# Kernel tuning notes

Hardware: AMD Instinct MI355X
Metric: run time of the kernel (lower is better)

Reference implementation:

```python
import jax, jax.numpy as jnp
import numpy as np

EPS = 1e-8
LAMBDA_LSE = 6.0
LAMBDA_SOFTMAX = 9.0
LEAKY_SLOPE = 0.1


def setup_inputs() -> dict:
    key = jax.random.key(0)
    k1, k2, k3 = jax.random.split(key, 3)
    images = jax.random.normal(k1, (128, 36, 512), dtype=jnp.float32)
    captions = jax.random.normal(k2, (64, 32, 512), dtype=jnp.float32)
    # caption lengths in [4, 32] so no caption is empty
    cap_lens = jax.random.randint(k3, (64,), 4, 33, dtype=jnp.int64)
    return {"images": images, "captions": captions, "cap_lens": cap_lens}


def reference(images, captions, cap_lens):
    """Vectorized xattn_score_t2i with raw_feature_norm='clipped_l2norm',
    agg_func='LogSumExp'. images: (I,R,D); captions: (C,L,D); cap_lens: (C,).
    Returns similarities (I, C), matching the torch per-caption loop.
    """
    C, L, D = captions.shape
    mask = jnp.arange(L)[None, :] < cap_lens[:, None]          # (C, L)

    # attn = bmm(context=images, query^T=words): (C, I, R, L)
    attn = jnp.einsum('ird,cld->cirl', images, captions)
    attn = jax.nn.leaky_relu(attn, LEAKY_SLOPE)
    # zero out padded words; equivalent to slicing caption to cap_len
    attn = attn * mask[:, None, None, :]
    # l2norm along the word dim (dim=2 of (I,R,L) in original)
    norm = jnp.sqrt(jnp.sum(attn * attn, axis=-1, keepdims=True)) + EPS
    attn = attn / norm

    # transpose -> (C, I, L, R); softmax over regions with smoothing
    attn = jnp.swapaxes(attn, -1, -2)
    attn = jax.nn.softmax(attn * LAMBDA_SOFTMAX, axis=-1)

    # weighted context: (C, I, L, D)
    wctx = jnp.einsum('cilr,ird->cild', attn, images)

    # cosine similarity between caption words and weighted context over D
    cap = captions[:, None, :, :]                               # (C, 1, L, D)
    num = jnp.sum(cap * wctx, axis=-1)                          # (C, I, L)
    den = (jnp.maximum(jnp.linalg.norm(cap, axis=-1), EPS) *
           jnp.maximum(jnp.linalg.norm(wctx, axis=-1), EPS))
    row_sim = num / den                                         # (C, I, L)

    # LogSumExp aggregation over valid words
    scores = jnp.where(mask[:, None, :], row_sim * LAMBDA_LSE, -jnp.inf)
    sims = jax.nn.logsumexp(scores, axis=-1) / LAMBDA_LSE       # (C, I)
    return sims.T                                               # (I, C)
```

## Files before the change

### kernel.cpp

```cpp
#include <hip/hip_runtime.h>
#include <math.h>

constexpr int In = 128, Rn = 36, Cn = 64, Ln = 32, Dn = 512;
constexpr int Mn = In * Rn;
constexpr int Nn = Cn * Ln;
constexpr size_t ABOFF = 0;
constexpr size_t BBOFF = (size_t)Mn * Dn / 2;
constexpr size_t GBOFF = BBOFF + (size_t)Nn * Dn / 2;
constexpr size_t CNOFF = GBOFF + (size_t)In * 48 * 64 / 2;
constexpr size_t WSFLOATS = CNOFF + (size_t)Cn * Ln;
constexpr float EPSf = 1e-8f, LLSE = 6.0f, LSM = 9.0f, SLOPE = 0.1f;

using short8 = __attribute__((ext_vector_type(8))) short;
using f32x4  = __attribute__((ext_vector_type(4))) float;

__device__ __forceinline__ float dot4(float4 a, float4 b) {
  return a.x * b.x + a.y * b.y + a.z * b.z + a.w * b.w;
}

__device__ __forceinline__ unsigned short f2bf(float x) {
  union { float f; unsigned u; } v; v.f = x;
  unsigned r = v.u + 0x7fffu + ((v.u >> 16) & 1u);
  return (unsigned short)(r >> 16);
}

__device__ __forceinline__ short8 pack8(float4 u, float4 v) {
  short8 s;
  s[0] = (short)f2bf(u.x); s[1] = (short)f2bf(u.y); s[2] = (short)f2bf(u.z); s[3] = (short)f2bf(u.w);
  s[4] = (short)f2bf(v.x); s[5] = (short)f2bf(v.y); s[6] = (short)f2bf(v.z); s[7] = (short)f2bf(v.w);
  return s;
}

extern "C" __global__ __launch_bounds__(256, 2)
void scan_pre(const float* __restrict__ images, const float* __restrict__ captions,
              float* __restrict__ ws)
{
  __shared__ unsigned short sI[48 * 520];
  const int tid = threadIdx.x;
  const int bx = blockIdx.x;
  const short8 z8 = {0, 0, 0, 0, 0, 0, 0, 0};

  if (bx < 128) {
    const int i = bx;
    const float* gi = images + (size_t)i * Rn * Dn;
    unsigned short* Ab = (unsigned short*)(ws + ABOFF) + (size_t)i * Rn * Dn;
    for (int q = 0; q < 9; ++q) {
      int ch = tid + q * 256;
      int r = ch >> 6, c8 = (ch & 63) * 8;
      float4 u = *reinterpret_cast<const float4*>(gi + r * Dn + c8);
      float4 v = *reinterpret_cast<const float4*>(gi + r * Dn + c8 + 4);
      short8 p = pack8(u, v);
      *reinterpret_cast<short8*>(Ab + r * Dn + c8) = p;
      *reinterpret_cast<short8*>(&sI[r * 520 + c8]) = p;
    }
    for (int q = 0; q < 3; ++q) {
      int ch = tid + q * 256;
      int r = 36 + (ch >> 6), c8 = (ch & 63) * 8;
      *reinterpret_cast<short8*>(&sI[r * 520 + c8]) = z8;
    }
    __syncthreads();
    const int lane = tid & 63, wv = tid >> 6;
    const int lr = lane & 15, lk = lane >> 4;
    unsigned short* gb = (unsigned short*)(ws + GBOFF) + (size_t)i * 48 * 64;
    for (int t = wv; t < 9; t += 4) {
      const int mt = t / 3, nt = t - mt * 3;
      f32x4 acc = {0.f, 0.f, 0.f, 0.f};
      for (int k = 0; k < 16; ++k) {
        short8 af = *reinterpret_cast<const short8*>(&sI[(mt * 16 + lr) * 520 + k * 32 + lk * 8]);
        short8 bf = *reinterpret_cast<const short8*>(&sI[(nt * 16 + lr) * 520 + k * 32 + lk * 8]);
        acc = __builtin_amdgcn_mfma_f32_16x16x32_bf16(af, bf, acc, 0, 0, 0);
      }
      #pragma unroll
      for (int j = 0; j < 4; ++j)
        gb[(mt * 16 + lk * 4 + j) * 64 + nt * 16 + lr] = f2bf(acc[j]);
    }
    if (tid < 96) {
      int r = tid >> 1, h = tid & 1;
      *reinterpret_cast<short8*>(gb + r * 64 + 48 + h * 8) = z8;
    }
    return;
  }
  if (bx < 640) {
    const int chunk = (bx - 128) * 256 + tid;
    const int c  = chunk >> 11;
    const int cc = chunk & 2047;
    const int ln = cc & 63;
    const int fc = cc >> 6;
    const int t  = fc >> 2;
    const int ks = (fc >> 1) & 1;
    const int y  = fc & 1;
    const int lr = ln & 15, lk = ln >> 4;
    const float* src = captions + ((size_t)c * Ln + y * 16 + lr) * Dn
                     + t * 64 + ks * 32 + lk * 8;
    float4 u = *reinterpret_cast<const float4*>(src);
    float4 v = *reinterpret_cast<const float4*>(src + 4);
    unsigned short* dst = (unsigned short*)(ws + BBOFF) + (size_t)chunk * 8;
    *reinterpret_cast<short8*>(dst) = pack8(u, v);
    return;
  }
  {
    const int c = bx - 640;
    const float* gc = captions + (size_t)c * Ln * Dn;
    const int l = tid >> 3, p = tid & 7;
    float s = 0.f;
    #pragma unroll
    for (int t = 0; t < 16; ++t) {
      float4 v = *reinterpret_cast<const float4*>(gc + l * Dn + p * 64 + t * 4);
      s += dot4(v, v);
    }
    s += __shfl_xor(s, 1, 64); s += __shfl_xor(s, 2, 64); s += __shfl_xor(s, 4, 64);
    if (p == 0) ws[CNOFF + c * Ln + l] = s;
  }
}

extern "C" __global__ __launch_bounds__(256, 3)
void scan_fused(const float* __restrict__ ws, const int* __restrict__ cap_lens,
                float* __restrict__ out)
{
  __shared__ unsigned short sA[48 * 520];
  const unsigned short* Ab = (const unsigned short*)(ws + ABOFF);
  const unsigned short* Bf = (const unsigned short*)(ws + BBOFF);
  const unsigned short* GbAll = (const unsigned short*)(ws + GBOFF);
  const float* cnArr = ws + CNOFF;

  const int tid = threadIdx.x;
  int bid = blockIdx.x;
  bid = (bid & 7) * 256 + (bid >> 3);
  const int ig = bid >> 4;
  const int cg = bid & 15;
  const int lane = tid & 63, wv = tid >> 6;
  const int lr = lane & 15, lk = lane >> 4;
  const int cap = cg * 4 + wv;
  const int len = cap_lens[cap];
  const short8 z8 = {0, 0, 0, 0, 0, 0, 0, 0};

  {
    const unsigned short* Abi = Ab + (size_t)ig * (Rn * Dn);
    #pragma unroll
    for (int q = 0; q < 9; ++q) {
      int ch = tid + q * 256;
      int r = ch >> 6, c8 = (ch & 63) * 8;
      *reinterpret_cast<short8*>(&sA[r * 520 + c8]) =
        *reinterpret_cast<const short8*>(Abi + r * Dn + c8);
    }
    #pragma unroll
    for (int q = 0; q < 3; ++q) {
      int ch = tid + q * 256;
      int r = 36 + (ch >> 6), c8 = (ch & 63) * 8;
      *reinterpret_cast<short8*>(&sA[r * 520 + c8]) = z8;
    }
  }
  __syncthreads();

  const unsigned short* gBp = Bf + (size_t)cap * 16384 + lane * 8;
  const unsigned short* rA = &sA[lr * 520 + lk * 8];

  f32x4 acc[3][2];
  #pragma unroll
  for (int x = 0; x < 3; ++x)
    #pragma unroll
    for (int y = 0; y < 2; ++y) acc[x][y] = {0.f, 0.f, 0.f, 0.f};

  short8 bc[4], bn[4];
  #pragma unroll
  for (int f = 0; f < 4; ++f)
    bc[f] = *reinterpret_cast<const short8*>(gBp + f * 512);

  #pragma unroll 2
  for (int t = 0; t < 8; ++t) {
    if (t < 7) {
      #pragma unroll
      for (int f = 0; f < 4; ++f)
        bn[f] = *reinterpret_cast<const short8*>(gBp + (t + 1) * 2048 + f * 512);
    }
    #pragma unroll
    for (int ks = 0; ks < 2; ++ks) {
      short8 af[3];
      #pragma unroll
      for (int x = 0; x < 3; ++x)
        af[x] = *reinterpret_cast<const short8*>(rA + x * 8320 + t * 64 + ks * 32);
      #pragma unroll
      for (int x = 0; x < 3; ++x)
        #pragma unroll
        for (int y = 0; y < 2; ++y)
          acc[x][y] = __builtin_amdgcn_mfma_f32_16x16x32_bf16(af[x], bc[ks * 2 + y], acc[x][y], 0, 0, 0);
    }
    if (t < 7) {
      #pragma unroll
      for (int f = 0; f < 4; ++f) bc[f] = bn[f];
    }
  }

  const unsigned short* Gb = GbAll + (size_t)ig * 48 * 64;
  short8 gfr[3][2];
  #pragma unroll
  for (int x = 0; x < 3; ++x)
    #pragma unroll
    for (int ks = 0; ks < 2; ++ks)
      gfr[x][ks] = *reinterpret_cast<const short8*>(Gb + (x * 16 + lr) * 64 + ks * 32 + lk * 8);
  const float cn0 = cnArr[cap * 32 + lr];
  const float cn1 = cnArr[cap * 32 + 16 + lr];

  float s[3][2][4];
  #pragma unroll
  for (int x = 0; x < 3; ++x)
    #pragma unroll
    for (int y = 0; y < 2; ++y) {
      const int l = y * 16 + lr;
      #pragma unroll
      for (int j = 0; j < 4; ++j) {
        float v = acc[x][y][j];
        v = v > 0.f ? v : SLOPE * v;
        if (l >= len) v = 0.f;
        s[x][y][j] = v;
      }
    }

  float zinv[3][4];
  #pragma unroll
  for (int x = 0; x < 3; ++x)
    #pragma unroll
    for (int j = 0; j < 4; ++j) {
      float t = s[x][0][j] * s[x][0][j] + s[x][1][j] * s[x][1][j];
      t += __shfl_xor(t, 1, 64); t += __shfl_xor(t, 2, 64);
      t += __shfl_xor(t, 4, 64); t += __shfl_xor(t, 8, 64);
      zinv[x][j] = LSM / (sqrtf(t) + EPSf);
    }

  const bool x2ok = (lk == 0);
  float mcol[2] = {-1e30f, -1e30f};
  #pragma unroll
  for (int x = 0; x < 3; ++x)
    #pragma unroll
    for (int y = 0; y < 2; ++y)
      #pragma unroll
      for (int j = 0; j < 4; ++j) {
        float zz = s[x][y][j] * zinv[x][j];
        s[x][y][j] = zz;
        if (x < 2 || x2ok) mcol[y] = fmaxf(mcol[y], zz);
      }
  #pragma unroll
  for (int y = 0; y < 2; ++y) {
    mcol[y] = fmaxf(mcol[y], __shfl_xor(mcol[y], 16, 64));
    mcol[y] = fmaxf(mcol[y], __shfl_xor(mcol[y], 32, 64));
  }

  float e[3][2][4];
  float esum[2] = {0.f, 0.f}, num[2] = {0.f, 0.f};
  #pragma unroll
  for (int x = 0; x < 3; ++x)
    #pragma unroll
    for (int y = 0; y < 2; ++y)
      #pragma unroll
      for (int j = 0; j < 4; ++j) {
        float ev = (x < 2 || x2ok) ? __expf(s[x][y][j] - mcol[y]) : 0.f;
        e[x][y][j] = ev;
        esum[y] += ev;
        num[y] = fmaf(ev, acc[x][y][j], num[y]);
      }
  #pragma unroll
  for (int y = 0; y < 2; ++y) {
    esum[y] += __shfl_xor(esum[y], 16, 64); esum[y] += __shfl_xor(esum[y], 32, 64);
    num[y]  += __shfl_xor(num[y], 16, 64);  num[y]  += __shfl_xor(num[y], 32, 64);
  }

  __syncthreads();
  unsigned short* ET = &sA[36 * 520 + wv * 1552];
  #pragma unroll
  for (int x = 0; x < 3; ++x)
    #pragma unroll
    for (int y = 0; y < 2; ++y)
      #pragma unroll
      for (int j = 0; j < 4; ++j)
        ET[(y * 16 + lr) * 48 + (x * 16 + lk * 4 + j)] = f2bf(e[x][y][j]);

  f32x4 vac[3][2];
  #pragma unroll
  for (int x = 0; x < 3; ++x)
    #pragma unroll
    for (int y = 0; y < 2; ++y) vac[x][y] = {0.f, 0.f, 0.f, 0.f};
  #pragma unroll
  for (int ks = 0; ks < 2; ++ks) {
    short8 efr[2];
    #pragma unroll
    for (int y = 0; y < 2; ++y)
      efr[y] = *reinterpret_cast<const short8*>(&ET[(y * 16 + lr) * 48 + ks * 32 + lk * 8]);
    #pragma unroll
    for (int x = 0; x < 3; ++x)
      #pragma unroll
      for (int y = 0; y < 2; ++y)
        vac[x][y] = __builtin_amdgcn_mfma_f32_16x16x32_bf16(gfr[x][ks], efr[y], vac[x][y], 0, 0, 0);
  }
  float wn[2] = {0.f, 0.f};
  #pragma unroll
  for (int x = 0; x < 3; ++x)
    #pragma unroll
    for (int y = 0; y < 2; ++y)
      #pragma unroll
      for (int j = 0; j < 4; ++j)
        wn[y] = fmaf(e[x][y][j], vac[x][y][j], wn[y]);
  #pragma unroll
  for (int y = 0; y < 2; ++y) {
    wn[y] += __shfl_xor(wn[y], 16, 64); wn[y] += __shfl_xor(wn[y], 32, 64);
  }

  float sc[2];
  #pragma unroll
  for (int y = 0; y < 2; ++y) {
    const int l = y * 16 + lr;
    const float cn = y ? cn1 : cn0;
    float inv = 1.f / esum[y];
    float nm = num[y] * inv;
    float w = fmaxf(wn[y], 0.f) * inv * inv;
    float den = fmaxf(sqrtf(cn), EPSf) * fmaxf(sqrtf(w), EPSf);
    sc[y] = (l < len) ? (nm / den) * LLSE : -INFINITY;
  }
  float mx = fmaxf(sc[0], sc[1]);
  mx = fmaxf(mx, __shfl_xor(mx, 1, 64)); mx = fmaxf(mx, __shfl_xor(mx, 2, 64));
  mx = fmaxf(mx, __shfl_xor(mx, 4, 64)); mx = fmaxf(mx, __shfl_xor(mx, 8, 64));
  float ex = __expf(sc[0] - mx) + __expf(sc[1] - mx);
  ex += __shfl_xor(ex, 1, 64); ex += __shfl_xor(ex, 2, 64);
  ex += __shfl_xor(ex, 4, 64); ex += __shfl_xor(ex, 8, 64);
  if (lane == 0) out[ig * Cn + cap] = (mx + __logf(ex)) / LLSE;
}

extern "C" void kernel_launch(void* const* d_in, const int* in_sizes, int n_in,
                              void* d_out, int out_size, void* d_ws, size_t ws_size,
                              hipStream_t stream) {
  const float* images   = (const float*)d_in[0];
  const float* captions = (const float*)d_in[1];
  const int*   cap_lens = (const int*)d_in[2];
  float* out = (float*)d_out;
  float* ws  = (float*)d_ws;
  if (ws_size < WSFLOATS * sizeof(float)) return;

  hipLaunchKernelGGL(scan_pre, dim3(704), dim3(256), 0, stream,
                     images, captions, ws);
  hipLaunchKernelGGL(scan_fused, dim3(In * 16), dim3(256), 0, stream,
                     ws, cap_lens, out);
}
```

Baseline: 42.95 us.

## Pre-swizzle image tiles into MFMA fragment layout and stream them from global

The pre-pass now writes image bf16 data in MFMA fragment order, zero-padded to 48 rows, instead of row-major. The fused kernel then loads A fragments directly from global memory into registers with a double-buffered prefetch, like the B operand, instead of staging a 48x520 tile in LDS. This removes the LDS fill, a block-wide barrier and the LDS reads, and cuts shared memory to a small per-wave E-transpose buffer, which may allow more resident blocks. The cost is more global and L2 traffic, since each of the four waves in a block loads the same A fragments, plus extra registers for the prefetch buffers.

```diff
diff --git a/kernel.cpp b/kernel.cpp
--- a/kernel.cpp
+++ b/kernel.cpp
@@ -4,8 +4,9 @@
 constexpr int In = 128, Rn = 36, Cn = 64, Ln = 32, Dn = 512;
 constexpr int Mn = In * Rn;
 constexpr int Nn = Cn * Ln;
-constexpr size_t ABOFF = 0;
-constexpr size_t BBOFF = (size_t)Mn * Dn / 2;
+constexpr size_t AFOFF = 0;
+constexpr size_t AFSZ  = (size_t)In * 24576 / 2;
+constexpr size_t BBOFF = AFSZ;
 constexpr size_t GBOFF = BBOFF + (size_t)Nn * Dn / 2;
 constexpr size_t CNOFF = GBOFF + (size_t)In * 48 * 64 / 2;
 constexpr size_t WSFLOATS = CNOFF + (size_t)Cn * Ln;
@@ -43,15 +44,12 @@
   if (bx < 128) {
     const int i = bx;
     const float* gi = images + (size_t)i * Rn * Dn;
-    unsigned short* Ab = (unsigned short*)(ws + ABOFF) + (size_t)i * Rn * Dn;
     for (int q = 0; q < 9; ++q) {
       int ch = tid + q * 256;
       int r = ch >> 6, c8 = (ch & 63) * 8;
       float4 u = *reinterpret_cast<const float4*>(gi + r * Dn + c8);
       float4 v = *reinterpret_cast<const float4*>(gi + r * Dn + c8 + 4);
-      short8 p = pack8(u, v);
-      *reinterpret_cast<short8*>(Ab + r * Dn + c8) = p;
-      *reinterpret_cast<short8*>(&sI[r * 520 + c8]) = p;
+      *reinterpret_cast<short8*>(&sI[r * 520 + c8]) = pack8(u, v);
     }
     for (int q = 0; q < 3; ++q) {
       int ch = tid + q * 256;
@@ -59,6 +57,20 @@
       *reinterpret_cast<short8*>(&sI[r * 520 + c8]) = z8;
     }
     __syncthreads();
+
+    unsigned short* af = (unsigned short*)(ws + AFOFF) + (size_t)i * 24576;
+    #pragma unroll
+    for (int q = 0; q < 12; ++q) {
+      int c = tid + q * 256;
+      int ln = c & 63, g = c >> 6;
+      int x = g % 3, ksq = g / 3;
+      int ks = ksq & 1, t = ksq >> 1;
+      int lr = ln & 15, lk = ln >> 4;
+      short8 v = *reinterpret_cast<const short8*>(
+          &sI[(x * 16 + lr) * 520 + t * 64 + ks * 32 + lk * 8]);
+      *reinterpret_cast<short8*>(af + (size_t)c * 8) = v;
+    }
+
     const int lane = tid & 63, wv = tid >> 6;
     const int lr = lane & 15, lk = lane >> 4;
     unsigned short* gb = (unsigned short*)(ws + GBOFF) + (size_t)i * 48 * 64;
@@ -66,9 +78,9 @@
       const int mt = t / 3, nt = t - mt * 3;
       f32x4 acc = {0.f, 0.f, 0.f, 0.f};
       for (int k = 0; k < 16; ++k) {
-        short8 af = *reinterpret_cast<const short8*>(&sI[(mt * 16 + lr) * 520 + k * 32 + lk * 8]);
-        short8 bf = *reinterpret_cast<const short8*>(&sI[(nt * 16 + lr) * 520 + k * 32 + lk * 8]);
-        acc = __builtin_amdgcn_mfma_f32_16x16x32_bf16(af, bf, acc, 0, 0, 0);
+        short8 af2 = *reinterpret_cast<const short8*>(&sI[(mt * 16 + lr) * 520 + k * 32 + lk * 8]);
+        short8 bf2 = *reinterpret_cast<const short8*>(&sI[(nt * 16 + lr) * 520 + k * 32 + lk * 8]);
+        acc = __builtin_amdgcn_mfma_f32_16x16x32_bf16(af2, bf2, acc, 0, 0, 0);
       }
       #pragma unroll
       for (int j = 0; j < 4; ++j)
@@ -117,8 +129,8 @@
 void scan_fused(const float* __restrict__ ws, const int* __restrict__ cap_lens,
                 float* __restrict__ out)
 {
-  __shared__ unsigned short sA[48 * 520];
-  const unsigned short* Ab = (const unsigned short*)(ws + ABOFF);
+  __shared__ unsigned short ETb[4][1568];
+  const unsigned short* AF = (const unsigned short*)(ws + AFOFF);
   const unsigned short* Bf = (const unsigned short*)(ws + BBOFF);
   const unsigned short* GbAll = (const unsigned short*)(ws + GBOFF);
   const float* cnArr = ws + CNOFF;
@@ -134,26 +146,11 @@
   const int len = cap_lens[cap];
   const short8 z8 = {0, 0, 0, 0, 0, 0, 0, 0};
 
-  {
-    const unsigned short* Abi = Ab + (size_t)ig * (Rn * Dn);
-    #pragma unroll
-    for (int q = 0; q < 9; ++q) {
-      int ch = tid + q * 256;
-      int r = ch >> 6, c8 = (ch & 63) * 8;
-      *reinterpret_cast<short8*>(&sA[r * 520 + c8]) =
-        *reinterpret_cast<const short8*>(Abi + r * Dn + c8);
-    }
-    #pragma unroll
-    for (int q = 0; q < 3; ++q) {
-      int ch = tid + q * 256;
-      int r = 36 + (ch >> 6), c8 = (ch & 63) * 8;
-      *reinterpret_cast<short8*>(&sA[r * 520 + c8]) = z8;
-    }
-  }
-  __syncthreads();
-
+  if (lane < 4)
+    *reinterpret_cast<short8*>(&ETb[wv][1536 + lane * 8]) = z8;
+
+  const unsigned short* gAf = AF + (size_t)ig * 24576 + lane * 8;
   const unsigned short* gBp = Bf + (size_t)cap * 16384 + lane * 8;
-  const unsigned short* rA = &sA[lr * 520 + lk * 8];
 
   f32x4 acc[3][2];
   #pragma unroll
@@ -161,7 +158,10 @@
     #pragma unroll
     for (int y = 0; y < 2; ++y) acc[x][y] = {0.f, 0.f, 0.f, 0.f};
 
-  short8 bc[4], bn[4];
+  short8 ac[6], an[6], bc[4], bn[4];
+  #pragma unroll
+  for (int f = 0; f < 6; ++f)
+    ac[f] = *reinterpret_cast<const short8*>(gAf + f * 512);
   #pragma unroll
   for (int f = 0; f < 4; ++f)
     bc[f] = *reinterpret_cast<const short8*>(gBp + f * 512);
@@ -170,22 +170,23 @@
   for (int t = 0; t < 8; ++t) {
     if (t < 7) {
       #pragma unroll
+      for (int f = 0; f < 6; ++f)
+        an[f] = *reinterpret_cast<const short8*>(gAf + ((t + 1) * 6 + f) * 512);
+      #pragma unroll
       for (int f = 0; f < 4; ++f)
-        bn[f] = *reinterpret_cast<const short8*>(gBp + (t + 1) * 2048 + f * 512);
-    }
-    #pragma unroll
-    for (int ks = 0; ks < 2; ++ks) {
-      short8 af[3];
-      #pragma unroll
-      for (int x = 0; x < 3; ++x)
-        af[x] = *reinterpret_cast<const short8*>(rA + x * 8320 + t * 64 + ks * 32);
+        bn[f] = *reinterpret_cast<const short8*>(gBp + ((t + 1) * 4 + f) * 512);
+    }
+    #pragma unroll
+    for (int ks = 0; ks < 2; ++ks)
       #pragma unroll
       for (int x = 0; x < 3; ++x)
         #pragma unroll
         for (int y = 0; y < 2; ++y)
-          acc[x][y] = __builtin_amdgcn_mfma_f32_16x16x32_bf16(af[x], bc[ks * 2 + y], acc[x][y], 0, 0, 0);
-    }
+          acc[x][y] = __builtin_amdgcn_mfma_f32_16x16x32_bf16(
+              ac[ks * 3 + x], bc[ks * 2 + y], acc[x][y], 0, 0, 0);
     if (t < 7) {
+      #pragma unroll
+      for (int f = 0; f < 6; ++f) ac[f] = an[f];
       #pragma unroll
       for (int f = 0; f < 4; ++f) bc[f] = bn[f];
     }
@@ -264,8 +265,7 @@
     num[y]  += __shfl_xor(num[y], 16, 64);  num[y]  += __shfl_xor(num[y], 32, 64);
   }
 
-  __syncthreads();
-  unsigned short* ET = &sA[36 * 520 + wv * 1552];
+  unsigned short* ET = ETb[wv];
   #pragma unroll
   for (int x = 0; x < 3; ++x)
     #pragma unroll
```

Measured after the change: 42.32 us. No clear change (-1.5%).
